# Kernel tuning notes

Measured on AMD Instinct MI355X. Metric: run time of the kernel, lower is better.

The kernel has to match this reference:

```python
import jax, jax.numpy as jnp
import numpy as np


def setup_inputs() -> dict:
    key = jax.random.key(0)
    k1, k2 = jax.random.split(key)
    set1 = jax.random.normal(k1, (8, 4096, 3), dtype=jnp.float32)
    set2 = jax.random.normal(k2, (8, 4096, 3), dtype=jnp.float32)
    return {"set1": set1, "set2": set2}


def reference(set1, set2):
    # set1: [b, n, d], set2: [b, m, d]
    n = set1.shape[1]
    x2 = jnp.sum(set1 * set1, axis=-1)            # [b, n]
    y2 = jnp.sum(set2 * set2, axis=-1)            # [b, m]
    xy = jnp.einsum('bnd,bmd->bnm', set1, set2)   # [b, n, m]
    d2 = x2[:, :, None] + y2[:, None, :] - 2.0 * xy
    dist = jnp.sqrt(jnp.maximum(d2, 0.0))         # torch.cdist(p=2)
    out_dist = jnp.min(dist, axis=2)              # [b, n]
    out_dist2 = jnp.min(dist, axis=1)             # [b, m]
    total = jnp.mean(out_dist) + jnp.mean(out_dist2)
    return total / n
```

## Files before the change

### kernel.cpp

```cpp
#include <hip/hip_runtime.h>
#include <math.h>
#include <float.h>


#define NTOT 65536
#define NPTS 4096

typedef __attribute__((ext_vector_type(8)))  short bf16x8;
typedef __attribute__((ext_vector_type(16))) float f32x16;

__device__ __forceinline__ unsigned short f2bf(float f) {
    union { float f; unsigned u; } v; v.f = f;
    return (unsigned short)((v.u + 0x7FFFu + ((v.u >> 16) & 1u)) >> 16);
}
__device__ __forceinline__ float bf2f(unsigned short h) {
    union { unsigned u; float f; } v; v.u = ((unsigned)h) << 16;
    return v.f;
}
__device__ __forceinline__ unsigned short m2(unsigned short h) {
    return f2bf(-2.0f * bf2f(h));
}
__device__ __forceinline__ unsigned pack2(unsigned a, unsigned b) {
    return (a & 0xFFFFu) | (b << 16);
}

__global__ __launch_bounds__(256)
void pack_pts(const float* __restrict__ set1, const float* __restrict__ set2,
              uint4* __restrict__ lo, uint4* __restrict__ hi,
              float* __restrict__ q2o)
{
    const int i = blockIdx.x * 256 + threadIdx.x;
    const float* __restrict__ src = (i < NTOT / 2) ? set1 : set2;
    const int idx = i & (NTOT / 2 - 1);
    const float x = src[3 * idx + 0];
    const float y = src[3 * idx + 1];
    const float z = src[3 * idx + 2];
    const unsigned short xh = f2bf(x), yh = f2bf(y), zh = f2bf(z);
    const unsigned short xl = f2bf(x - bf2f(xh));
    const unsigned short yl = f2bf(y - bf2f(yh));
    const unsigned short zl = f2bf(z - bf2f(zh));
    const float p2 = fmaf(x, x, fmaf(y, y, z * z));
    const unsigned short pa = f2bf(p2);
    const float r1 = p2 - bf2f(pa);
    const unsigned short pb = f2bf(r1);
    const unsigned short pc = f2bf(r1 - bf2f(pb));
    lo[i] = make_uint4(pack2(xh, yh), pack2(zh, xl), pack2(yl, zl), pack2(xh, yh));
    hi[i] = make_uint4(pack2(zh, xl), pack2(yl, zl), pack2(pa, pb), pack2(pc, 0));
    q2o[i] = p2;
}

__device__ __forceinline__ float fold16(const f32x16 c, float m) {
    m = fminf(fminf(c[0],  c[1]),  m);
    m = fminf(fminf(c[2],  c[3]),  m);
    m = fminf(fminf(c[4],  c[5]),  m);
    m = fminf(fminf(c[6],  c[7]),  m);
    m = fminf(fminf(c[8],  c[9]),  m);
    m = fminf(fminf(c[10], c[11]), m);
    m = fminf(fminf(c[12], c[13]), m);
    m = fminf(fminf(c[14], c[15]), m);
    return m;
}

__global__ __launch_bounds__(512, 4)
void chamfer_main(const uint4* __restrict__ lo, const uint4* __restrict__ hi,
                  const float* __restrict__ q2arr, float* __restrict__ out)
{
    __shared__ float part[8][128];

    const int blk = blockIdx.x;
    const int dir = blk >> 8;
    const int rem = blk & 255;
    const int b   = rem >> 5;
    const int qc  = rem & 31;

    const int qBase  = dir * (NTOT / 2) + b * NPTS + qc * 128;
    const int dbBase = (1 - dir) * (NTOT / 2) + b * NPTS;

    const int t    = threadIdx.x;
    const int lane = t & 63;
    const int w    = t >> 6;
    const int col  = lane & 31;
    const int half = lane >> 5;

    const uint4* __restrict__ qsrc = half ? hi : lo;
    bf16x8 Bf[4];
    #pragma unroll
    for (int j = 0; j < 4; ++j) {
        const uint4 sv = qsrc[qBase + j * 32 + col];
        const unsigned short s0 = sv.x & 0xFFFF, s1 = sv.x >> 16;
        const unsigned short s2 = sv.y & 0xFFFF, s3 = sv.y >> 16;
        const unsigned short s4 = sv.z & 0xFFFF;
        uint4 bv;
        if (!half) {
            const unsigned short a0 = m2(s0), a1 = m2(s1), a2 = m2(s2);
            bv = make_uint4(pack2(a0, a1), pack2(a2, a0),
                            pack2(a1, a2), pack2(m2(s3), m2(s4)));
        } else {
            const unsigned short a3 = m2(s3);
            const unsigned one = 0x3F80u;
            bv = make_uint4(pack2(a3, m2(s1)), pack2(m2(s2), a3),
                            pack2(one, one), pack2(one, 0));
        }
        Bf[j] = *reinterpret_cast<bf16x8*>(&bv);
    }

    const f32x16 zero16 = {0,0,0,0,0,0,0,0,0,0,0,0,0,0,0,0};
    float dmin0 = FLT_MAX, dmin1 = FLT_MAX, dmin2 = FLT_MAX, dmin3 = FLT_MAX;

    const uint4* __restrict__ Abase = (half ? hi : lo) + (dbBase + w * 512 + col);

    #pragma unroll 4
    for (int pt = 0; pt < 16; ++pt) {
        const bf16x8 a = *reinterpret_cast<const bf16x8*>(Abase + pt * 32);
        f32x16 c;
        c = __builtin_amdgcn_mfma_f32_32x32x16_bf16(a, Bf[0], zero16, 0, 0, 0);
        dmin0 = fold16(c, dmin0);
        c = __builtin_amdgcn_mfma_f32_32x32x16_bf16(a, Bf[1], zero16, 0, 0, 0);
        dmin1 = fold16(c, dmin1);
        c = __builtin_amdgcn_mfma_f32_32x32x16_bf16(a, Bf[2], zero16, 0, 0, 0);
        dmin2 = fold16(c, dmin2);
        c = __builtin_amdgcn_mfma_f32_32x32x16_bf16(a, Bf[3], zero16, 0, 0, 0);
        dmin3 = fold16(c, dmin3);
    }

    float dmin[4] = {dmin0, dmin1, dmin2, dmin3};
    #pragma unroll
    for (int j = 0; j < 4; ++j) {
        const float v = fminf(dmin[j], __shfl_xor(dmin[j], 32));
        if (!half) part[w][j * 32 + col] = v;
    }
    __syncthreads();

    float dist = 0.0f;
    if (t < 128) {
        float m = part[0][t];
        #pragma unroll
        for (int ww = 1; ww < 8; ++ww)
            m = fminf(m, part[ww][t]);
        const float q2 = q2arr[qBase + t];
        dist = sqrtf(fmaxf(q2 + m, 0.0f));
    }
    #pragma unroll
    for (int off = 32; off > 0; off >>= 1)
        dist += __shfl_down(dist, off);
    if (t < 128 && (t & 63) == 0)
        atomicAdd(out, dist * (1.0f / 134217728.0f));
}

extern "C" void kernel_launch(void* const* d_in, const int* in_sizes, int n_in,
                              void* d_out, int out_size, void* d_ws, size_t ws_size,
                              hipStream_t stream) {
    const float* s1 = (const float*)d_in[0];
    const float* s2 = (const float*)d_in[1];
    float* out = (float*)d_out;

    char* ws = (char*)d_ws;
    uint4* lo = (uint4*)ws;
    uint4* hi = (uint4*)(ws + (1u << 20));
    float* q2 = (float*)(ws + (2u << 20));

    hipMemsetAsync(out, 0, sizeof(float), stream);
    pack_pts<<<dim3(NTOT / 256), dim3(256), 0, stream>>>(s1, s2, lo, hi, q2);
    chamfer_main<<<dim3(512), dim3(512), 0, stream>>>(lo, hi, q2, out);
}
```

Baseline: 79.10 us.

## Fuse point packing into chamfer kernel with fp16 split and LDS staging

Removes the separate packing kernel: each block now converts its 4096 database points to fp16 hi/lo fragments directly into LDS, and builds query fragments from raw floats. Switches the MFMA from bf16 to fp16 with a two-term split, dropping one correction term for the norm, and masks the A operand per half-wave instead of storing two global arrays. This saves a kernel launch and the global workspace round trip, at the cost of redundant per-block conversion work (each DB batch is converted by 32 blocks) and 64KB of LDS per block, which caps occupancy below the requested launch bounds. The fp16 split also has different range and precision behaviour than bf16.

```diff
diff --git a/kernel.cpp b/kernel.cpp
--- a/kernel.cpp
+++ b/kernel.cpp
@@ -3,50 +3,16 @@
 #include <float.h>
 
 
-#define NTOT 65536
 #define NPTS 4096
 
-typedef __attribute__((ext_vector_type(8)))  short bf16x8;
-typedef __attribute__((ext_vector_type(16))) float f32x16;
+typedef __attribute__((ext_vector_type(8)))  _Float16 f16x8;
+typedef __attribute__((ext_vector_type(16))) float    f32x16;
 
-__device__ __forceinline__ unsigned short f2bf(float f) {
-    union { float f; unsigned u; } v; v.f = f;
-    return (unsigned short)((v.u + 0x7FFFu + ((v.u >> 16) & 1u)) >> 16);
+static __device__ __forceinline__ unsigned h2u(_Float16 h) {
+    return (unsigned)__builtin_bit_cast(unsigned short, h);
 }
-__device__ __forceinline__ float bf2f(unsigned short h) {
-    union { unsigned u; float f; } v; v.u = ((unsigned)h) << 16;
-    return v.f;
-}
-__device__ __forceinline__ unsigned short m2(unsigned short h) {
-    return f2bf(-2.0f * bf2f(h));
-}
-__device__ __forceinline__ unsigned pack2(unsigned a, unsigned b) {
+static __device__ __forceinline__ unsigned pack2(unsigned a, unsigned b) {
     return (a & 0xFFFFu) | (b << 16);
-}
-
-__global__ __launch_bounds__(256)
-void pack_pts(const float* __restrict__ set1, const float* __restrict__ set2,
-              uint4* __restrict__ lo, uint4* __restrict__ hi,
-              float* __restrict__ q2o)
-{
-    const int i = blockIdx.x * 256 + threadIdx.x;
-    const float* __restrict__ src = (i < NTOT / 2) ? set1 : set2;
-    const int idx = i & (NTOT / 2 - 1);
-    const float x = src[3 * idx + 0];
-    const float y = src[3 * idx + 1];
-    const float z = src[3 * idx + 2];
-    const unsigned short xh = f2bf(x), yh = f2bf(y), zh = f2bf(z);
-    const unsigned short xl = f2bf(x - bf2f(xh));
-    const unsigned short yl = f2bf(y - bf2f(yh));
-    const unsigned short zl = f2bf(z - bf2f(zh));
-    const float p2 = fmaf(x, x, fmaf(y, y, z * z));
-    const unsigned short pa = f2bf(p2);
-    const float r1 = p2 - bf2f(pa);
-    const unsigned short pb = f2bf(r1);
-    const unsigned short pc = f2bf(r1 - bf2f(pb));
-    lo[i] = make_uint4(pack2(xh, yh), pack2(zh, xl), pack2(yl, zl), pack2(xh, yh));
-    hi[i] = make_uint4(pack2(zh, xl), pack2(yl, zl), pack2(pa, pb), pack2(pc, 0));
-    q2o[i] = p2;
 }
 
 __device__ __forceinline__ float fold16(const f32x16 c, float m) {
@@ -62,10 +28,11 @@
 }
 
 __global__ __launch_bounds__(512, 4)
-void chamfer_main(const uint4* __restrict__ lo, const uint4* __restrict__ hi,
-                  const float* __restrict__ q2arr, float* __restrict__ out)
+void chamfer_fused(const float* __restrict__ set1,
+                   const float* __restrict__ set2,
+                   float* __restrict__ out)
 {
-    __shared__ float part[8][128];
+    __shared__ uint4 frag[NPTS];
 
     const int blk = blockIdx.x;
     const int dir = blk >> 8;
@@ -73,71 +40,102 @@
     const int b   = rem >> 5;
     const int qc  = rem & 31;
 
-    const int qBase  = dir * (NTOT / 2) + b * NPTS + qc * 128;
-    const int dbBase = (1 - dir) * (NTOT / 2) + b * NPTS;
+    const float* __restrict__ Q  = (dir ? set2 : set1) + (size_t)b * NPTS * 3;
+    const float* __restrict__ DB = (dir ? set1 : set2) + (size_t)b * NPTS * 3;
 
     const int t    = threadIdx.x;
     const int lane = t & 63;
     const int w    = t >> 6;
     const int col  = lane & 31;
     const int half = lane >> 5;
+    const int qbase = qc * 128;
 
-    const uint4* __restrict__ qsrc = half ? hi : lo;
-    bf16x8 Bf[4];
+    #pragma unroll
+    for (int k = 0; k < 8; ++k) {
+        const int p = t + 512 * k;
+        const float x = DB[3 * p + 0];
+        const float y = DB[3 * p + 1];
+        const float z = DB[3 * p + 2];
+        const _Float16 hx = (_Float16)x, hy = (_Float16)y, hz = (_Float16)z;
+        const _Float16 lx = (_Float16)(x - (float)hx);
+        const _Float16 ly = (_Float16)(y - (float)hy);
+        const _Float16 lz = (_Float16)(z - (float)hz);
+        const float p2 = fmaf(x, x, fmaf(y, y, z * z));
+        const _Float16 p2h = (_Float16)p2;
+        const _Float16 p2l = (_Float16)(p2 - (float)p2h);
+        frag[p] = make_uint4(pack2(h2u(hx),  h2u(hy)),
+                             pack2(h2u(hz),  h2u(lx)),
+                             pack2(h2u(ly),  h2u(lz)),
+                             pack2(h2u(p2h), h2u(p2l)));
+    }
+
+    f16x8 Bf[4];
     #pragma unroll
     for (int j = 0; j < 4; ++j) {
-        const uint4 sv = qsrc[qBase + j * 32 + col];
-        const unsigned short s0 = sv.x & 0xFFFF, s1 = sv.x >> 16;
-        const unsigned short s2 = sv.y & 0xFFFF, s3 = sv.y >> 16;
-        const unsigned short s4 = sv.z & 0xFFFF;
+        const float* qp = Q + (size_t)(qbase + j * 32 + col) * 3;
+        const float qx = qp[0], qy = qp[1], qz = qp[2];
+        const _Float16 hx = (_Float16)qx, hy = (_Float16)qy, hz = (_Float16)qz;
         uint4 bv;
         if (!half) {
-            const unsigned short a0 = m2(s0), a1 = m2(s1), a2 = m2(s2);
-            bv = make_uint4(pack2(a0, a1), pack2(a2, a0),
-                            pack2(a1, a2), pack2(m2(s3), m2(s4)));
+            const unsigned mx = h2u((_Float16)(-2.0f * (float)hx));
+            const unsigned my = h2u((_Float16)(-2.0f * (float)hy));
+            const unsigned mz = h2u((_Float16)(-2.0f * (float)hz));
+            const unsigned one = 0x3C00u;
+            bv = make_uint4(pack2(mx, my), pack2(mz, mx),
+                            pack2(my, mz), pack2(one, one));
         } else {
-            const unsigned short a3 = m2(s3);
-            const unsigned one = 0x3F80u;
-            bv = make_uint4(pack2(a3, m2(s1)), pack2(m2(s2), a3),
-                            pack2(one, one), pack2(one, 0));
+            const unsigned mx = h2u((_Float16)(-2.0f * (qx - (float)hx)));
+            const unsigned my = h2u((_Float16)(-2.0f * (qy - (float)hy)));
+            const unsigned mz = h2u((_Float16)(-2.0f * (qz - (float)hz)));
+            bv = make_uint4(pack2(mx, my), pack2(mz, 0), 0u, 0u);
         }
-        Bf[j] = *reinterpret_cast<bf16x8*>(&bv);
+        Bf[j] = __builtin_bit_cast(f16x8, bv);
     }
 
-    const f32x16 zero16 = {0,0,0,0,0,0,0,0,0,0,0,0,0,0,0,0};
-    float dmin0 = FLT_MAX, dmin1 = FLT_MAX, dmin2 = FLT_MAX, dmin3 = FLT_MAX;
+    __syncthreads();
 
-    const uint4* __restrict__ Abase = (half ? hi : lo) + (dbBase + w * 512 + col);
+    const unsigned mY  = half ? 0x0000FFFFu : 0xFFFFFFFFu;
+    const unsigned mZW = half ? 0u          : 0xFFFFFFFFu;
+    const uint4* __restrict__ fb = frag + w * 512 + col;
 
-    #pragma unroll 4
+    const f32x16 z16 = {0,0,0,0,0,0,0,0,0,0,0,0,0,0,0,0};
+    float dm0 = FLT_MAX, dm1 = FLT_MAX, dm2 = FLT_MAX, dm3 = FLT_MAX;
+
+    uint4 u = fb[0];
     for (int pt = 0; pt < 16; ++pt) {
-        const bf16x8 a = *reinterpret_cast<const bf16x8*>(Abase + pt * 32);
-        f32x16 c;
-        c = __builtin_amdgcn_mfma_f32_32x32x16_bf16(a, Bf[0], zero16, 0, 0, 0);
-        dmin0 = fold16(c, dmin0);
-        c = __builtin_amdgcn_mfma_f32_32x32x16_bf16(a, Bf[1], zero16, 0, 0, 0);
-        dmin1 = fold16(c, dmin1);
-        c = __builtin_amdgcn_mfma_f32_32x32x16_bf16(a, Bf[2], zero16, 0, 0, 0);
-        dmin2 = fold16(c, dmin2);
-        c = __builtin_amdgcn_mfma_f32_32x32x16_bf16(a, Bf[3], zero16, 0, 0, 0);
-        dmin3 = fold16(c, dmin3);
+        uint4 un = u;
+        if (pt < 15) un = fb[(pt + 1) * 32];
+        const uint4 am = make_uint4(u.x, u.y & mY, u.z & mZW, u.w & mZW);
+        const f16x8 av = __builtin_bit_cast(f16x8, am);
+        f32x16 c0 = __builtin_amdgcn_mfma_f32_32x32x16_f16(av, Bf[0], z16, 0, 0, 0);
+        f32x16 c1 = __builtin_amdgcn_mfma_f32_32x32x16_f16(av, Bf[1], z16, 0, 0, 0);
+        dm0 = fold16(c0, dm0);
+        c0 = __builtin_amdgcn_mfma_f32_32x32x16_f16(av, Bf[2], z16, 0, 0, 0);
+        dm1 = fold16(c1, dm1);
+        c1 = __builtin_amdgcn_mfma_f32_32x32x16_f16(av, Bf[3], z16, 0, 0, 0);
+        dm2 = fold16(c0, dm2);
+        dm3 = fold16(c1, dm3);
+        u = un;
     }
 
-    float dmin[4] = {dmin0, dmin1, dmin2, dmin3};
+    float dmin[4] = {dm0, dm1, dm2, dm3};
+    __syncthreads();
+    float* part = (float*)frag;
     #pragma unroll
     for (int j = 0; j < 4; ++j) {
         const float v = fminf(dmin[j], __shfl_xor(dmin[j], 32));
-        if (!half) part[w][j * 32 + col] = v;
+        if (!half) part[w * 128 + j * 32 + col] = v;
     }
     __syncthreads();
 
     float dist = 0.0f;
     if (t < 128) {
-        float m = part[0][t];
+        float m = part[t];
         #pragma unroll
         for (int ww = 1; ww < 8; ++ww)
-            m = fminf(m, part[ww][t]);
-        const float q2 = q2arr[qBase + t];
+            m = fminf(m, part[ww * 128 + t]);
+        const float* qp = Q + (size_t)(qbase + t) * 3;
+        const float q2 = fmaf(qp[0], qp[0], fmaf(qp[1], qp[1], qp[2] * qp[2]));
         dist = sqrtf(fmaxf(q2 + m, 0.0f));
     }
     #pragma unroll
@@ -154,12 +152,6 @@
     const float* s2 = (const float*)d_in[1];
     float* out = (float*)d_out;
 
-    char* ws = (char*)d_ws;
-    uint4* lo = (uint4*)ws;
-    uint4* hi = (uint4*)(ws + (1u << 20));
-    float* q2 = (float*)(ws + (2u << 20));
-
     hipMemsetAsync(out, 0, sizeof(float), stream);
-    pack_pts<<<dim3(NTOT / 256), dim3(256), 0, stream>>>(s1, s2, lo, hi, q2);
-    chamfer_main<<<dim3(512), dim3(512), 0, stream>>>(lo, hi, q2, out);
+    chamfer_fused<<<dim3(512), dim3(512), 0, stream>>>(s1, s2, out);
 }
```

New measurement: 73.82 us. 6.7% less time.
